# Performance work log

Hardware: AMD Instinct MI355X
Metric: run time of the kernel (lower is better)

The kernel has to match this reference:

```python
import jax, jax.numpy as jnp
import numpy as np

D = 1024  # bilinear_dim
IN_A = 1024
IN_B = 1024

def setup_inputs() -> dict:
    key = jax.random.key(0)
    ks = jax.random.split(key, 8)
    B, La, Lb = 64, 256, 256
    sa = 1.0 / np.sqrt(IN_A)
    sb = 1.0 / np.sqrt(IN_B)
    sd = 1.0 / np.sqrt(D)
    return {
        "a": jax.random.normal(ks[0], (B, La, IN_A), dtype=jnp.float32),
        "b": jax.random.normal(ks[1], (B, Lb, IN_B), dtype=jnp.float32),
        "Wa": jax.random.uniform(ks[2], (IN_A, D), jnp.float32, -sa, sa),
        "ba": jax.random.uniform(ks[3], (D,), jnp.float32, -sa, sa),
        "Wb": jax.random.uniform(ks[4], (IN_B, D), jnp.float32, -sb, sb),
        "bb": jax.random.uniform(ks[5], (D,), jnp.float32, -sb, sb),
        "w": jax.random.uniform(ks[6], (D,), jnp.float32, -sd, sd),
        "wbias": jax.random.uniform(ks[7], (), jnp.float32, -sd, sd),
    }

def reference(a, b, Wa, ba, Wb, bb, w, wbias):
    # Linear projections (dropout inactive at inference)
    pa = a @ Wa + ba          # (B, La, D)
    pb = b @ Wb + bb          # (B, Lb, D)
    # Fused bilinear score: sum_d w[d]*pa[b,i,d]*pb[b,j,d] + wbias
    # (equivalent to materializing (B,La,Lb,D) outer product then Linear(D->1))
    scores = jnp.einsum('bid,bjd->bij', pa * w, pb) + wbias  # (B, La, Lb)
    B, La, Lb = scores.shape
    norm = jax.nn.softmax(scores.reshape(B, La * Lb), axis=1)
    return norm.reshape(B, La, Lb)
```

## Files before the change

### kernel.cpp

```cpp
#include <hip/hip_runtime.h>
#include <hip/hip_bf16.h>

typedef __attribute__((ext_vector_type(8))) short bf16x8;
typedef __attribute__((ext_vector_type(4))) float f32x4;

#define K_DIM 1024
#define M_PROJ 16384
#define NBATCH 64
#define SEQ 256

static __device__ inline unsigned short bf16_bits(float f) {
    __hip_bfloat16 h = __float2bfloat16(f);
    return *reinterpret_cast<unsigned short*>(&h);
}

#define GLOAD16(g, l) __builtin_amdgcn_global_load_lds(                          \
    (__attribute__((address_space(1))) void*)(g),                                \
    (__attribute__((address_space(3))) void*)(l), 16, 0, 0)

__global__ __launch_bounds__(256) void prep(const float* __restrict__ Wa,
                                            const float* __restrict__ Wb,
                                            const float* __restrict__ w,
                                            const float* __restrict__ ba,
                                            const float* __restrict__ bb,
                                            unsigned short* __restrict__ Waw,
                                            unsigned short* __restrict__ Wb16,
                                            float* __restrict__ u,
                                            float* __restrict__ v,
                                            float* __restrict__ c,
                                            unsigned int* __restrict__ counters)
{
    __shared__ float psum[4];
    const int blk = blockIdx.x;
    const int t = threadIdx.x;

    if (blk < 1024) {
        const int isA = (blk < 512);
        const int r  = (isA ? blk : blk - 512) * 2 + (t >> 7);
        const int c8 = (t & 127) * 8;
        const float* in  = isA ? Wa : Wb;
        const float* bv  = isA ? bb : ba;
        unsigned short* o = isA ? Waw : Wb16;

        const float* xp = &in[(size_t)r * K_DIM + c8];
        float4 v0 = *(const float4*)xp;
        float4 v1 = *(const float4*)(xp + 4);
        float4 w0 = *(const float4*)&w[c8];
        float4 w1 = *(const float4*)&w[c8 + 4];
        float4 b0 = *(const float4*)&bv[c8];
        float4 b1 = *(const float4*)&bv[c8 + 4];

        float part = v0.x * w0.x * b0.x + v0.y * w0.y * b0.y
                   + v0.z * w0.z * b0.z + v0.w * w0.w * b0.w
                   + v1.x * w1.x * b1.x + v1.y * w1.y * b1.y
                   + v1.z * w1.z * b1.z + v1.w * w1.w * b1.w;

        if (isA) {
            v0.x *= w0.x; v0.y *= w0.y; v0.z *= w0.z; v0.w *= w0.w;
            v1.x *= w1.x; v1.y *= w1.y; v1.z *= w1.z; v1.w *= w1.w;
        }
        unsigned short uo[8];
        uo[0] = bf16_bits(v0.x); uo[1] = bf16_bits(v0.y); uo[2] = bf16_bits(v0.z); uo[3] = bf16_bits(v0.w);
        uo[4] = bf16_bits(v1.x); uo[5] = bf16_bits(v1.y); uo[6] = bf16_bits(v1.z); uo[7] = bf16_bits(v1.w);
        *reinterpret_cast<uint4*>(&o[(size_t)r * K_DIM + c8]) = *reinterpret_cast<uint4*>(uo);

#pragma unroll
        for (int off = 32; off; off >>= 1) part += __shfl_down(part, off);
        if ((t & 63) == 0) psum[t >> 6] = part;
        __syncthreads();
        if ((t & 127) == 0) {
            const float s = psum[t >> 6] + psum[(t >> 6) + 1];
            if (isA) u[r] = s; else v[r] = s;
        }
        return;
    }
    if (blk == 1025) {
        if (t < NBATCH) counters[t] = 0u;
        return;
    }
    const int d0 = t * 4;
    float4 ww = *(const float4*)&w[d0];
    float4 b1 = *(const float4*)&ba[d0];
    float4 b2 = *(const float4*)&bb[d0];
    float part = ww.x * b1.x * b2.x + ww.y * b1.y * b2.y
               + ww.z * b1.z * b2.z + ww.w * b1.w * b2.w;
#pragma unroll
    for (int off = 32; off; off >>= 1) part += __shfl_down(part, off);
    if ((t & 63) == 0) psum[t >> 6] = part;
    __syncthreads();
    if (t == 0) *c = (psum[0] + psum[1]) + (psum[2] + psum[3]);
}

__global__ __launch_bounds__(256) void conv_rows(const float* __restrict__ X,
                                                 const float* __restrict__ dvec,
                                                 unsigned short* __restrict__ out,
                                                 float* __restrict__ rowdot)
{
    __shared__ float psum[4];
    const int t = threadIdx.x;
    const int r = blockIdx.x * 2 + (t >> 7);
    const int c8 = (t & 127) * 8;

    const float* xp = &X[(size_t)r * K_DIM + c8];
    float4 v0 = *(const float4*)xp;
    float4 v1 = *(const float4*)(xp + 4);
    float4 u0 = *(const float4*)&dvec[c8];
    float4 u1 = *(const float4*)&dvec[c8 + 4];
    float part = v0.x * u0.x + v0.y * u0.y + v0.z * u0.z + v0.w * u0.w
               + v1.x * u1.x + v1.y * u1.y + v1.z * u1.z + v1.w * u1.w;

    unsigned short uo[8];
    uo[0] = bf16_bits(v0.x); uo[1] = bf16_bits(v0.y); uo[2] = bf16_bits(v0.z); uo[3] = bf16_bits(v0.w);
    uo[4] = bf16_bits(v1.x); uo[5] = bf16_bits(v1.y); uo[6] = bf16_bits(v1.z); uo[7] = bf16_bits(v1.w);
    *reinterpret_cast<uint4*>(&out[(size_t)r * K_DIM + c8]) = *reinterpret_cast<uint4*>(uo);

#pragma unroll
    for (int off = 32; off; off >>= 1) part += __shfl_down(part, off);
    if ((t & 63) == 0) psum[t >> 6] = part;
    __syncthreads();
    if ((t & 127) == 0) rowdot[r] = psum[(t >> 6)] + psum[(t >> 6) + 1];
}

__global__ __launch_bounds__(256) void mt_gemm(const __hip_bfloat16* __restrict__ Wb16,
                                               const __hip_bfloat16* __restrict__ Waw,
                                               unsigned short* __restrict__ Mt)
{
    __shared__ __align__(16) unsigned short As[128][32];
    __shared__ __align__(16) unsigned short Bs[128][32];

    const int tid  = threadIdx.x;
    const int lane = tid & 63;
    const int wave = tid >> 6;
    const int q0 = blockIdx.x * 128;
    const int p0 = blockIdx.y * 128;
    const int wr = (wave >> 1) * 64;
    const int wc = (wave & 1) * 64;

    const __hip_bfloat16* Arow = Wb16 + (size_t)q0 * K_DIM;
    const __hip_bfloat16* Brow = Waw + (size_t)p0 * K_DIM;

    f32x4 acc[4][4];
#pragma unroll
    for (int i = 0; i < 4; ++i)
#pragma unroll
        for (int j = 0; j < 4; ++j) acc[i][j] = f32x4{0.f, 0.f, 0.f, 0.f};

    const int lrow = lane & 15;
    const int kq   = (lane >> 4) * 8;

    for (int k0 = 0; k0 < K_DIM; k0 += 32) {
        __syncthreads();
#pragma unroll
        for (int it = 0; it < 2; ++it) {
            const int chunk = (it * 4 + wave) * 64 + lane;
            const int row = chunk >> 2;
            const int col = (chunk & 3) * 8;
            GLOAD16(Arow + (size_t)row * K_DIM + k0 + col,
                    reinterpret_cast<char*>(&As[0][0]) + (it * 4 + wave) * 1024);
        }
#pragma unroll
        for (int it = 0; it < 2; ++it) {
            const int chunk = (it * 4 + wave) * 64 + lane;
            const int row = chunk >> 2;
            const int col = (chunk & 3) * 8;
            GLOAD16(Brow + (size_t)row * K_DIM + k0 + col,
                    reinterpret_cast<char*>(&Bs[0][0]) + (it * 4 + wave) * 1024);
        }
        __syncthreads();

        bf16x8 af[4], bfr[4];
#pragma unroll
        for (int f = 0; f < 4; ++f) {
            af[f]  = *reinterpret_cast<const bf16x8*>(&As[wr + f * 16 + lrow][kq]);
            bfr[f] = *reinterpret_cast<const bf16x8*>(&Bs[wc + f * 16 + lrow][kq]);
        }
#pragma unroll
        for (int i = 0; i < 4; ++i)
#pragma unroll
            for (int j = 0; j < 4; ++j)
                acc[i][j] = __builtin_amdgcn_mfma_f32_16x16x32_bf16(bfr[j], af[i], acc[i][j], 0, 0, 0);
    }

#pragma unroll
    for (int ii = 0; ii < 4; ++ii) {
        const int q = q0 + wr + ii * 16 + lrow;
#pragma unroll
        for (int jj = 0; jj < 4; ++jj) {
            const int pb = p0 + wc + jj * 16 + (lane >> 4) * 4;
            unsigned short uo[4];
            uo[0] = bf16_bits(acc[ii][jj][0]);
            uo[1] = bf16_bits(acc[ii][jj][1]);
            uo[2] = bf16_bits(acc[ii][jj][2]);
            uo[3] = bf16_bits(acc[ii][jj][3]);
            *(ushort4*)&Mt[(size_t)q * K_DIM + pb] = *(ushort4*)uo;
        }
    }
}

__global__ __launch_bounds__(512, 2) void proj_gemm256(
    const __hip_bfloat16* __restrict__ A,
    const __hip_bfloat16* __restrict__ Wt,
    __hip_bfloat16* __restrict__ out)
{
    __shared__ __align__(16) unsigned short lds[2][4][128 * 64];

    const int tid  = threadIdx.x;
    const int lane = tid & 63;
    const int w    = tid >> 6;
    const int wr   = w >> 2;
    const int wc   = w & 3;
    const int m0 = blockIdx.x * 256;
    const int n0 = blockIdx.y * 256;

    const int c1 = w * 128 + lane, c2 = c1 + 64;
    const int r1 = c1 >> 3, r2 = c2 >> 3;
    const int k1 = (c1 & 7) ^ (r1 & 7);
    const int k2 = (c2 & 7) ^ (r2 & 7);

    const int lrow = lane & 15;
    const int kq0  = (((lane >> 4) + 0) ^ (lane & 7)) * 16;
    const int kq1  = (((lane >> 4) + 4) ^ (lane & 7)) * 16;

#define STG(SRC, RB, KB, BUF, REG)                                               \
    {                                                                            \
        GLOAD16((SRC) + (size_t)((RB) + r1) * K_DIM + (KB) + k1 * 8,             \
                (char*)(&lds[BUF][REG][0]) + w * 2048);                          \
        GLOAD16((SRC) + (size_t)((RB) + r2) * K_DIM + (KB) + k2 * 8,             \
                (char*)(&lds[BUF][REG][0]) + w * 2048 + 1024);                   \
    }

    f32x4 acc[8][4];
#pragma unroll
    for (int i = 0; i < 8; ++i)
#pragma unroll
        for (int j = 0; j < 4; ++j) acc[i][j] = f32x4{0.f, 0.f, 0.f, 0.f};

    STG(A,  m0,       0, 0, 0); STG(A,  m0 + 128,  0, 0, 1);
    STG(Wt, n0,       0, 0, 2); STG(Wt, n0 + 128,  0, 0, 3);
    STG(A,  m0,      64, 1, 0); STG(A,  m0 + 128, 64, 1, 1);
    asm volatile("s_waitcnt vmcnt(4)" ::: "memory");
    __builtin_amdgcn_sched_barrier(0);
    __builtin_amdgcn_s_barrier();

#define KTILE(CUR, NXT, T)                                                       \
    {                                                                            \
        const int kb1 = (((T) + 1) & 15) << 6;                                   \
        const int kb2 = (((T) + 2) & 15) << 6;                                   \
        const char* Ab = (const char*)(&lds[CUR][wr][0]);                        \
        const char* Bb = (const char*)(&lds[CUR][2 + (wc >> 1)][0])              \
                         + (wc & 1) * 8192;                                      \
        bf16x8 af[4][2], bfr[4][2];                                              \
        _Pragma("unroll")                                                        \
        for (int mi = 0; mi < 4; ++mi) {                                         \
            af[mi][0] = *(const bf16x8*)(Ab + mi * 2048 + lrow * 128 + kq0);     \
            af[mi][1] = *(const bf16x8*)(Ab + mi * 2048 + lrow * 128 + kq1);     \
        }                                                                        \
        _Pragma("unroll")                                                        \
        for (int nj = 0; nj < 2; ++nj) {                                         \
            bfr[nj][0] = *(const bf16x8*)(Bb + nj * 2048 + lrow * 128 + kq0);    \
            bfr[nj][1] = *(const bf16x8*)(Bb + nj * 2048 + lrow * 128 + kq1);    \
        }                                                                        \
        STG(Wt, n0, kb1, NXT, 2);                                                \
        __builtin_amdgcn_sched_barrier(0);                                       \
        __builtin_amdgcn_s_barrier();                                            \
        asm volatile("s_waitcnt lgkmcnt(0)" ::: "memory");                       \
        __builtin_amdgcn_sched_barrier(0);                                       \
        __builtin_amdgcn_s_setprio(1);                                           \
        _Pragma("unroll")                                                        \
        for (int mi = 0; mi < 4; ++mi)                                           \
            _Pragma("unroll")                                                    \
            for (int nj = 0; nj < 2; ++nj) {                                     \
                acc[mi][nj] = __builtin_amdgcn_mfma_f32_16x16x32_bf16(           \
                    bfr[nj][0], af[mi][0], acc[mi][nj], 0, 0, 0);                \
                acc[mi][nj] = __builtin_amdgcn_mfma_f32_16x16x32_bf16(           \
                    bfr[nj][1], af[mi][1], acc[mi][nj], 0, 0, 0);                \
            }                                                                    \
        __builtin_amdgcn_s_setprio(0);                                           \
        __builtin_amdgcn_sched_barrier(0);                                       \
        __builtin_amdgcn_s_barrier();                                            \
        _Pragma("unroll")                                                        \
        for (int nj = 2; nj < 4; ++nj) {                                         \
            bfr[nj][0] = *(const bf16x8*)(Bb + nj * 2048 + lrow * 128 + kq0);    \
            bfr[nj][1] = *(const bf16x8*)(Bb + nj * 2048 + lrow * 128 + kq1);    \
        }                                                                        \
        STG(Wt, n0 + 128, kb1, NXT, 3);                                          \
        __builtin_amdgcn_sched_barrier(0);                                       \
        __builtin_amdgcn_s_barrier();                                            \
        asm volatile("s_waitcnt lgkmcnt(0)" ::: "memory");                       \
        __builtin_amdgcn_sched_barrier(0);                                       \
        __builtin_amdgcn_s_setprio(1);                                           \
        _Pragma("unroll")                                                        \
        for (int mi = 0; mi < 4; ++mi)                                           \
            _Pragma("unroll")                                                    \
            for (int nj = 2; nj < 4; ++nj) {                                     \
                acc[mi][nj] = __builtin_amdgcn_mfma_f32_16x16x32_bf16(           \
                    bfr[nj][0], af[mi][0], acc[mi][nj], 0, 0, 0);                \
                acc[mi][nj] = __builtin_amdgcn_mfma_f32_16x16x32_bf16(           \
                    bfr[nj][1], af[mi][1], acc[mi][nj], 0, 0, 0);                \
            }                                                                    \
        __builtin_amdgcn_s_setprio(0);                                           \
        __builtin_amdgcn_sched_barrier(0);                                       \
        __builtin_amdgcn_s_barrier();                                            \
        _Pragma("unroll")                                                        \
        for (int mi = 0; mi < 4; ++mi) {                                         \
            af[mi][0] = *(const bf16x8*)(Ab + 8192 + mi * 2048 + lrow * 128 + kq0);\
            af[mi][1] = *(const bf16x8*)(Ab + 8192 + mi * 2048 + lrow * 128 + kq1);\
        }                                                                        \
        __builtin_amdgcn_sched_barrier(0);                                       \
        __builtin_amdgcn_s_barrier();                                            \
        asm volatile("s_waitcnt lgkmcnt(0)" ::: "memory");                       \
        __builtin_amdgcn_sched_barrier(0);                                       \
        __builtin_amdgcn_s_setprio(1);                                           \
        _Pragma("unroll")                                                        \
        for (int mi = 0; mi < 4; ++mi)                                           \
            _Pragma("unroll")                                                    \
            for (int nj = 0; nj < 2; ++nj) {                                     \
                acc[4 + mi][nj] = __builtin_amdgcn_mfma_f32_16x16x32_bf16(       \
                    bfr[nj][0], af[mi][0], acc[4 + mi][nj], 0, 0, 0);            \
                acc[4 + mi][nj] = __builtin_amdgcn_mfma_f32_16x16x32_bf16(       \
                    bfr[nj][1], af[mi][1], acc[4 + mi][nj], 0, 0, 0);            \
            }                                                                    \
        __builtin_amdgcn_s_setprio(0);                                           \
        __builtin_amdgcn_sched_barrier(0);                                       \
        __builtin_amdgcn_s_barrier();                                            \
        STG(A, m0,       kb2, CUR, 0);                                           \
        STG(A, m0 + 128, kb2, CUR, 1);                                           \
        __builtin_amdgcn_sched_barrier(0);                                       \
        __builtin_amdgcn_s_barrier();                                            \
        __builtin_amdgcn_s_setprio(1);                                           \
        _Pragma("unroll")                                                        \
        for (int mi = 0; mi < 4; ++mi)                                           \
            _Pragma("unroll")                                                    \
            for (int nj = 2; nj < 4; ++nj) {                                     \
                acc[4 + mi][nj] = __builtin_amdgcn_mfma_f32_16x16x32_bf16(       \
                    bfr[nj][0], af[mi][0], acc[4 + mi][nj], 0, 0, 0);            \
                acc[4 + mi][nj] = __builtin_amdgcn_mfma_f32_16x16x32_bf16(       \
                    bfr[nj][1], af[mi][1], acc[4 + mi][nj], 0, 0, 0);            \
            }                                                                    \
        __builtin_amdgcn_s_setprio(0);                                           \
        asm volatile("s_waitcnt vmcnt(4)" ::: "memory");                         \
        __builtin_amdgcn_sched_barrier(0);                                       \
        __builtin_amdgcn_s_barrier();                                            \
    }

    for (int tt = 0; tt < 8; ++tt) {
        const int t0 = tt * 2;
        KTILE(0, 1, t0);
        KTILE(1, 0, t0 + 1);
    }
#undef KTILE
#undef STG

    asm volatile("s_waitcnt vmcnt(0)" ::: "memory");
    __builtin_amdgcn_sched_barrier(0);
    __builtin_amdgcn_s_barrier();
    char* eb = (char*)(&lds[0][0][0]);
#pragma unroll
    for (int mi8 = 0; mi8 < 8; ++mi8) {
        const int ml = wr * 128 + (mi8 >> 2) * 64 + (mi8 & 3) * 16 + lrow;
#pragma unroll
        for (int nj = 0; nj < 4; ++nj) {
            const int nl = wc * 64 + nj * 16 + (lane >> 4) * 4;
            unsigned short uo[4];
            uo[0] = bf16_bits(acc[mi8][nj][0]);
            uo[1] = bf16_bits(acc[mi8][nj][1]);
            uo[2] = bf16_bits(acc[mi8][nj][2]);
            uo[3] = bf16_bits(acc[mi8][nj][3]);
            const int vv = nl >> 3;
            *(ushort4*)(eb + ml * 512 + ((vv ^ (ml & 7)) * 16) + ((nl >> 2) & 1) * 8)
                = *(ushort4*)uo;
        }
    }
    __syncthreads();
#pragma unroll
    for (int p = 0; p < 2; ++p) {
        const int ml = p * 128 + (tid >> 2);
#pragma unroll
        for (int it = 0; it < 8; ++it) {
            const int vv = it * 4 + (tid & 3);
            uint4 val = *(const uint4*)(eb + ml * 512 + ((vv ^ (ml & 7)) * 16));
            *(uint4*)&out[(size_t)(m0 + ml) * K_DIM + n0 + vv * 8] = val;
        }
    }
}

__global__ __launch_bounds__(256) void score_gemm(const __hip_bfloat16* __restrict__ T,
                                                  const __hip_bfloat16* __restrict__ Bbf,
                                                  const float* __restrict__ alpha,
                                                  const float* __restrict__ beta,
                                                  const float* __restrict__ cptr,
                                                  const float* __restrict__ wbias,
                                                  float* __restrict__ out,
                                                  float* __restrict__ partials,
                                                  unsigned int* __restrict__ counters)
{
    __shared__ __align__(16) unsigned short As[128][32];
    __shared__ __align__(16) unsigned short Bs[128][32];
    __shared__ float psum[4];
    __shared__ float inv_s;

    const int tid  = threadIdx.x;
    const int lane = tid & 63;
    const int wave = tid >> 6;
    const int b  = blockIdx.z;
    const int i0 = blockIdx.x * 128;
    const int j0 = blockIdx.y * 128;
    const int wr = (wave >> 1) * 64;
    const int wc = (wave & 1) * 64;

    const __hip_bfloat16* Arow = T + (size_t)(b * SEQ + i0) * K_DIM;
    const __hip_bfloat16* Brow = Bbf + (size_t)(b * SEQ + j0) * K_DIM;

    f32x4 acc[4][4];
#pragma unroll
    for (int i = 0; i < 4; ++i)
#pragma unroll
        for (int j = 0; j < 4; ++j) acc[i][j] = f32x4{0.f, 0.f, 0.f, 0.f};

    const int lrow = lane & 15;
    const int kq   = (lane >> 4) * 8;

    for (int k0 = 0; k0 < K_DIM; k0 += 32) {
        __syncthreads();
#pragma unroll
        for (int it = 0; it < 2; ++it) {
            const int chunk = (it * 4 + wave) * 64 + lane;
            const int row = chunk >> 2;
            const int col = (chunk & 3) * 8;
            GLOAD16(Arow + (size_t)row * K_DIM + k0 + col,
                    reinterpret_cast<char*>(&As[0][0]) + (it * 4 + wave) * 1024);
        }
#pragma unroll
        for (int it = 0; it < 2; ++it) {
            const int chunk = (it * 4 + wave) * 64 + lane;
            const int row = chunk >> 2;
            const int col = (chunk & 3) * 8;
            GLOAD16(Brow + (size_t)row * K_DIM + k0 + col,
                    reinterpret_cast<char*>(&Bs[0][0]) + (it * 4 + wave) * 1024);
        }
        __syncthreads();

        bf16x8 af[4], bfr[4];
#pragma unroll
        for (int f = 0; f < 4; ++f) {
            af[f]  = *reinterpret_cast<const bf16x8*>(&As[wr + f * 16 + lrow][kq]);
            bfr[f] = *reinterpret_cast<const bf16x8*>(&Bs[wc + f * 16 + lrow][kq]);
        }
#pragma unroll
        for (int i = 0; i < 4; ++i)
#pragma unroll
            for (int j = 0; j < 4; ++j)
                acc[i][j] = __builtin_amdgcn_mfma_f32_16x16x32_bf16(bfr[j], af[i], acc[i][j], 0, 0, 0);
    }

    const float cwb = *cptr + *wbias;
    float lsum = 0.f;
#pragma unroll
    for (int ii = 0; ii < 4; ++ii) {
        const int i = i0 + wr + ii * 16 + lrow;
        const float av = alpha[b * SEQ + i] + cwb;
#pragma unroll
        for (int jj = 0; jj < 4; ++jj) {
            const int jb = j0 + wc + jj * 16 + (lane >> 4) * 4;
            const float4 bv = *(const float4*)&beta[b * SEQ + jb];
            acc[ii][jj][0] = __expf(acc[ii][jj][0] + av + bv.x);
            acc[ii][jj][1] = __expf(acc[ii][jj][1] + av + bv.y);
            acc[ii][jj][2] = __expf(acc[ii][jj][2] + av + bv.z);
            acc[ii][jj][3] = __expf(acc[ii][jj][3] + av + bv.w);
            lsum += (acc[ii][jj][0] + acc[ii][jj][1]) + (acc[ii][jj][2] + acc[ii][jj][3]);
        }
    }
#pragma unroll
    for (int off = 32; off; off >>= 1) lsum += __shfl_down(lsum, off);
    if (lane == 0) psum[wave] = lsum;
    __syncthreads();

    const int pidx = b * 4 + blockIdx.x * 2 + blockIdx.y;
    if (tid == 0) {
        const float my = (psum[0] + psum[1]) + (psum[2] + psum[3]);
        __hip_atomic_store(&partials[pidx], my, __ATOMIC_RELEASE, __HIP_MEMORY_SCOPE_AGENT);
        __hip_atomic_fetch_add(&counters[b], 1u, __ATOMIC_RELEASE, __HIP_MEMORY_SCOPE_AGENT);
        while (__hip_atomic_load(&counters[b], __ATOMIC_ACQUIRE, __HIP_MEMORY_SCOPE_AGENT) < 4u) {}
        const float p0 = __hip_atomic_load(&partials[b * 4 + 0], __ATOMIC_RELAXED, __HIP_MEMORY_SCOPE_AGENT);
        const float p1 = __hip_atomic_load(&partials[b * 4 + 1], __ATOMIC_RELAXED, __HIP_MEMORY_SCOPE_AGENT);
        const float p2 = __hip_atomic_load(&partials[b * 4 + 2], __ATOMIC_RELAXED, __HIP_MEMORY_SCOPE_AGENT);
        const float p3 = __hip_atomic_load(&partials[b * 4 + 3], __ATOMIC_RELAXED, __HIP_MEMORY_SCOPE_AGENT);
        inv_s = 1.0f / (((p0 + p1) + p2) + p3);
    }
    __syncthreads();
    const float inv = inv_s;

#pragma unroll
    for (int ii = 0; ii < 4; ++ii) {
        const int i = i0 + wr + ii * 16 + lrow;
#pragma unroll
        for (int jj = 0; jj < 4; ++jj) {
            const int jb = j0 + wc + jj * 16 + (lane >> 4) * 4;
            float4 e;
            e.x = acc[ii][jj][0] * inv;
            e.y = acc[ii][jj][1] * inv;
            e.z = acc[ii][jj][2] * inv;
            e.w = acc[ii][jj][3] * inv;
            *(float4*)&out[(size_t)b * (SEQ * SEQ) + (size_t)i * SEQ + jb] = e;
        }
    }
}

extern "C" void kernel_launch(void* const* d_in, const int* in_sizes, int n_in,
                              void* d_out, int out_size, void* d_ws, size_t ws_size,
                              hipStream_t stream)
{
    const float* a     = (const float*)d_in[0];
    const float* b     = (const float*)d_in[1];
    const float* Wa    = (const float*)d_in[2];
    const float* ba    = (const float*)d_in[3];
    const float* Wb    = (const float*)d_in[4];
    const float* bb    = (const float*)d_in[5];
    const float* w     = (const float*)d_in[6];
    const float* wbias = (const float*)d_in[7];
    float* out = (float*)d_out;

    char* wsb = (char*)d_ws;
    unsigned short* Waw   = (unsigned short*)(wsb);
    unsigned short* Wb16  = (unsigned short*)(wsb + (size_t)2097152);
    unsigned short* Mt    = (unsigned short*)(wsb + (size_t)4194304);
    float* u              = (float*)(wsb + (size_t)6291456);
    float* v              = (float*)(wsb + (size_t)6291456 + 4096);
    float* c              = (float*)(wsb + (size_t)6291456 + 8192);
    float* alpha          = (float*)(wsb + (size_t)6291456 + 16384);
    float* beta           = (float*)(wsb + (size_t)6291456 + 16384 + 65536);
    float* partials       = (float*)(wsb + (size_t)6291456 + 16384 + 131072);
    unsigned int* counters= (unsigned int*)(wsb + (size_t)6291456 + 16384 + 131072 + 1024);
    unsigned short* ab16  = (unsigned short*)(wsb + (size_t)8388608);
    unsigned short* Tbuf  = (unsigned short*)(wsb + (size_t)41943040);

    prep<<<1026, 256, 0, stream>>>(Wa, Wb, w, ba, bb, Waw, Wb16, u, v, c, counters);
    mt_gemm<<<dim3(8, 8), 256, 0, stream>>>((const __hip_bfloat16*)Wb16,
                                            (const __hip_bfloat16*)Waw, Mt);
    conv_rows<<<M_PROJ / 2, 256, 0, stream>>>(a, u, ab16, alpha);
    const dim3 pgrid(M_PROJ / 256, K_DIM / 256);
    proj_gemm256<<<pgrid, 512, 0, stream>>>((const __hip_bfloat16*)ab16,
                                            (const __hip_bfloat16*)Mt,
                                            (__hip_bfloat16*)Tbuf);
    conv_rows<<<M_PROJ / 2, 256, 0, stream>>>(b, v, ab16, beta);
    const dim3 sgrid(SEQ / 128, SEQ / 128, NBATCH);
    score_gemm<<<sgrid, 256, 0, stream>>>((const __hip_bfloat16*)Tbuf,
                                          (const __hip_bfloat16*)ab16,
                                          alpha, beta, c, wbias, out, partials, counters);
}
```

Measured before the change: 130.2 us.

## Replace intra-kernel spin barrier with separate normalize kernel and smaller score tiles

Score GEMM now uses 64x64 tiles (16 blocks per batch, 4096 total) and writes unnormalized exp scores plus per-block partial sums. A new normalize kernel then reads all partials per batch and rescales the 16 MB output in place. This removes the atomic counter spin-wait, which required all blocks of a batch to be co-resident, and the counter reset in prep. The cost is an extra read and write pass over the output, plus lower data reuse from the smaller GEMM tiles.

```diff
diff --git a/kernel.cpp b/kernel.cpp
--- a/kernel.cpp
+++ b/kernel.cpp
@@ -27,8 +27,7 @@
                                             unsigned short* __restrict__ Wb16,
                                             float* __restrict__ u,
                                             float* __restrict__ v,
-                                            float* __restrict__ c,
-                                            unsigned int* __restrict__ counters)
+                                            float* __restrict__ c)
 {
     __shared__ float psum[4];
     const int blk = blockIdx.x;
@@ -72,10 +71,6 @@
             const float s = psum[t >> 6] + psum[(t >> 6) + 1];
             if (isA) u[r] = s; else v[r] = s;
         }
-        return;
-    }
-    if (blk == 1025) {
-        if (t < NBATCH) counters[t] = 0u;
         return;
     }
     const int d0 = t * 4;
@@ -391,118 +386,101 @@
                                                   const float* __restrict__ cptr,
                                                   const float* __restrict__ wbias,
                                                   float* __restrict__ out,
-                                                  float* __restrict__ partials,
-                                                  unsigned int* __restrict__ counters)
-{
-    __shared__ __align__(16) unsigned short As[128][32];
-    __shared__ __align__(16) unsigned short Bs[128][32];
+                                                  float* __restrict__ partials)
+{
+    __shared__ __align__(16) unsigned short As[64][32];
+    __shared__ __align__(16) unsigned short Bs[64][32];
     __shared__ float psum[4];
-    __shared__ float inv_s;
 
     const int tid  = threadIdx.x;
     const int lane = tid & 63;
     const int wave = tid >> 6;
     const int b  = blockIdx.z;
-    const int i0 = blockIdx.x * 128;
-    const int j0 = blockIdx.y * 128;
-    const int wr = (wave >> 1) * 64;
-    const int wc = (wave & 1) * 64;
+    const int i0 = blockIdx.x * 64;
+    const int j0 = blockIdx.y * 64;
+    const int wr = (wave >> 1) * 32;
+    const int wc = (wave & 1) * 32;
 
     const __hip_bfloat16* Arow = T + (size_t)(b * SEQ + i0) * K_DIM;
     const __hip_bfloat16* Brow = Bbf + (size_t)(b * SEQ + j0) * K_DIM;
 
-    f32x4 acc[4][4];
-#pragma unroll
-    for (int i = 0; i < 4; ++i)
-#pragma unroll
-        for (int j = 0; j < 4; ++j) acc[i][j] = f32x4{0.f, 0.f, 0.f, 0.f};
+    f32x4 acc[2][2];
+#pragma unroll
+    for (int i = 0; i < 2; ++i)
+#pragma unroll
+        for (int j = 0; j < 2; ++j) acc[i][j] = f32x4{0.f, 0.f, 0.f, 0.f};
 
     const int lrow = lane & 15;
     const int kq   = (lane >> 4) * 8;
+    const int srow = tid >> 2;
+    const int scol = (tid & 3) * 8;
 
     for (int k0 = 0; k0 < K_DIM; k0 += 32) {
         __syncthreads();
-#pragma unroll
-        for (int it = 0; it < 2; ++it) {
-            const int chunk = (it * 4 + wave) * 64 + lane;
-            const int row = chunk >> 2;
-            const int col = (chunk & 3) * 8;
-            GLOAD16(Arow + (size_t)row * K_DIM + k0 + col,
-                    reinterpret_cast<char*>(&As[0][0]) + (it * 4 + wave) * 1024);
-        }
-#pragma unroll
-        for (int it = 0; it < 2; ++it) {
-            const int chunk = (it * 4 + wave) * 64 + lane;
-            const int row = chunk >> 2;
-            const int col = (chunk & 3) * 8;
-            GLOAD16(Brow + (size_t)row * K_DIM + k0 + col,
-                    reinterpret_cast<char*>(&Bs[0][0]) + (it * 4 + wave) * 1024);
-        }
+        GLOAD16(Arow + (size_t)srow * K_DIM + k0 + scol,
+                reinterpret_cast<char*>(&As[0][0]) + wave * 1024);
+        GLOAD16(Brow + (size_t)srow * K_DIM + k0 + scol,
+                reinterpret_cast<char*>(&Bs[0][0]) + wave * 1024);
         __syncthreads();
 
-        bf16x8 af[4], bfr[4];
-#pragma unroll
-        for (int f = 0; f < 4; ++f) {
+        bf16x8 af[2], bfr[2];
+#pragma unroll
+        for (int f = 0; f < 2; ++f) {
             af[f]  = *reinterpret_cast<const bf16x8*>(&As[wr + f * 16 + lrow][kq]);
             bfr[f] = *reinterpret_cast<const bf16x8*>(&Bs[wc + f * 16 + lrow][kq]);
         }
 #pragma unroll
-        for (int i = 0; i < 4; ++i)
-#pragma unroll
-            for (int j = 0; j < 4; ++j)
+        for (int i = 0; i < 2; ++i)
+#pragma unroll
+            for (int j = 0; j < 2; ++j)
                 acc[i][j] = __builtin_amdgcn_mfma_f32_16x16x32_bf16(bfr[j], af[i], acc[i][j], 0, 0, 0);
     }
 
     const float cwb = *cptr + *wbias;
     float lsum = 0.f;
 #pragma unroll
-    for (int ii = 0; ii < 4; ++ii) {
+    for (int ii = 0; ii < 2; ++ii) {
         const int i = i0 + wr + ii * 16 + lrow;
         const float av = alpha[b * SEQ + i] + cwb;
 #pragma unroll
-        for (int jj = 0; jj < 4; ++jj) {
+        for (int jj = 0; jj < 2; ++jj) {
             const int jb = j0 + wc + jj * 16 + (lane >> 4) * 4;
             const float4 bv = *(const float4*)&beta[b * SEQ + jb];
-            acc[ii][jj][0] = __expf(acc[ii][jj][0] + av + bv.x);
-            acc[ii][jj][1] = __expf(acc[ii][jj][1] + av + bv.y);
-            acc[ii][jj][2] = __expf(acc[ii][jj][2] + av + bv.z);
-            acc[ii][jj][3] = __expf(acc[ii][jj][3] + av + bv.w);
-            lsum += (acc[ii][jj][0] + acc[ii][jj][1]) + (acc[ii][jj][2] + acc[ii][jj][3]);
+            float4 e;
+            e.x = __expf(acc[ii][jj][0] + av + bv.x);
+            e.y = __expf(acc[ii][jj][1] + av + bv.y);
+            e.z = __expf(acc[ii][jj][2] + av + bv.z);
+            e.w = __expf(acc[ii][jj][3] + av + bv.w);
+            lsum += (e.x + e.y) + (e.z + e.w);
+            *(float4*)&out[(size_t)b * (SEQ * SEQ) + (size_t)i * SEQ + jb] = e;
         }
     }
 #pragma unroll
     for (int off = 32; off; off >>= 1) lsum += __shfl_down(lsum, off);
     if (lane == 0) psum[wave] = lsum;
     __syncthreads();
-
-    const int pidx = b * 4 + blockIdx.x * 2 + blockIdx.y;
-    if (tid == 0) {
-        const float my = (psum[0] + psum[1]) + (psum[2] + psum[3]);
-        __hip_atomic_store(&partials[pidx], my, __ATOMIC_RELEASE, __HIP_MEMORY_SCOPE_AGENT);
-        __hip_atomic_fetch_add(&counters[b], 1u, __ATOMIC_RELEASE, __HIP_MEMORY_SCOPE_AGENT);
-        while (__hip_atomic_load(&counters[b], __ATOMIC_ACQUIRE, __HIP_MEMORY_SCOPE_AGENT) < 4u) {}
-        const float p0 = __hip_atomic_load(&partials[b * 4 + 0], __ATOMIC_RELAXED, __HIP_MEMORY_SCOPE_AGENT);
-        const float p1 = __hip_atomic_load(&partials[b * 4 + 1], __ATOMIC_RELAXED, __HIP_MEMORY_SCOPE_AGENT);
-        const float p2 = __hip_atomic_load(&partials[b * 4 + 2], __ATOMIC_RELAXED, __HIP_MEMORY_SCOPE_AGENT);
-        const float p3 = __hip_atomic_load(&partials[b * 4 + 3], __ATOMIC_RELAXED, __HIP_MEMORY_SCOPE_AGENT);
-        inv_s = 1.0f / (((p0 + p1) + p2) + p3);
-    }
-    __syncthreads();
-    const float inv = inv_s;
-
-#pragma unroll
-    for (int ii = 0; ii < 4; ++ii) {
-        const int i = i0 + wr + ii * 16 + lrow;
-#pragma unroll
-        for (int jj = 0; jj < 4; ++jj) {
-            const int jb = j0 + wc + jj * 16 + (lane >> 4) * 4;
-            float4 e;
-            e.x = acc[ii][jj][0] * inv;
-            e.y = acc[ii][jj][1] * inv;
-            e.z = acc[ii][jj][2] * inv;
-            e.w = acc[ii][jj][3] * inv;
-            *(float4*)&out[(size_t)b * (SEQ * SEQ) + (size_t)i * SEQ + jb] = e;
-        }
+    if (tid == 0)
+        partials[b * 16 + blockIdx.x * 4 + blockIdx.y] =
+            (psum[0] + psum[1]) + (psum[2] + psum[3]);
+}
+
+__global__ __launch_bounds__(1024) void normalize_k(float* __restrict__ s,
+                                                    const float* __restrict__ partials)
+{
+    const int b    = blockIdx.x >> 2;
+    const int part = blockIdx.x & 3;
+    float sum = 0.f;
+#pragma unroll
+    for (int i = 0; i < 16; ++i) sum += partials[b * 16 + i];
+    const float inv = 1.0f / sum;
+    float4* p4 = reinterpret_cast<float4*>(s + (size_t)b * (SEQ * SEQ));
+    const int base = part * 4096;
+#pragma unroll
+    for (int it = 0; it < 4; ++it) {
+        const int i = base + it * 1024 + threadIdx.x;
+        float4 v = p4[i];
+        v.x *= inv; v.y *= inv; v.z *= inv; v.w *= inv;
+        p4[i] = v;
     }
 }
 
@@ -530,11 +508,10 @@
     float* alpha          = (float*)(wsb + (size_t)6291456 + 16384);
     float* beta           = (float*)(wsb + (size_t)6291456 + 16384 + 65536);
     float* partials       = (float*)(wsb + (size_t)6291456 + 16384 + 131072);
-    unsigned int* counters= (unsigned int*)(wsb + (size_t)6291456 + 16384 + 131072 + 1024);
     unsigned short* ab16  = (unsigned short*)(wsb + (size_t)8388608);
     unsigned short* Tbuf  = (unsigned short*)(wsb + (size_t)41943040);
 
-    prep<<<1026, 256, 0, stream>>>(Wa, Wb, w, ba, bb, Waw, Wb16, u, v, c, counters);
+    prep<<<1025, 256, 0, stream>>>(Wa, Wb, w, ba, bb, Waw, Wb16, u, v, c);
     mt_gemm<<<dim3(8, 8), 256, 0, stream>>>((const __hip_bfloat16*)Wb16,
                                             (const __hip_bfloat16*)Waw, Mt);
     conv_rows<<<M_PROJ / 2, 256, 0, stream>>>(a, u, ab16, alpha);
@@ -543,8 +520,9 @@
                                             (const __hip_bfloat16*)Mt,
                                             (__hip_bfloat16*)Tbuf);
     conv_rows<<<M_PROJ / 2, 256, 0, stream>>>(b, v, ab16, beta);
-    const dim3 sgrid(SEQ / 128, SEQ / 128, NBATCH);
+    const dim3 sgrid(SEQ / 64, SEQ / 64, NBATCH);
     score_gemm<<<sgrid, 256, 0, stream>>>((const __hip_bfloat16*)Tbuf,
                                           (const __hip_bfloat16*)ab16,
-                                          alpha, beta, c, wbias, out, partials, counters);
-}
+                                          alpha, beta, c, wbias, out, partials);
+    normalize_k<<<NBATCH * 4, 1024, 0, stream>>>(out, partials);
+}
```

New measurement: 134.5 us. 1.03x slower.
